# Kernel optimization log

Measured on AMD Instinct MI355X. Metric: run time of the kernel, lower is better.

## Reference

```python
import jax, jax.numpy as jnp
import numpy as np

B, CIN, D = 4096, 4, 8
EPS = 1e-5
NEG_SLOPE = 0.01


def _conv3d(x, w):
    # x: [B,C,D,H,W], w: [kD,kH,kW,Cin,Cout]
    return jax.lax.conv_general_dilated(
        x, w, window_strides=(1, 1, 1), padding='SAME',
        dimension_numbers=('NCDHW', 'DHWIO', 'NCDHW'))


def _bn(x, gamma, beta, mean, var):
    s = (1, -1) + (1,) * (x.ndim - 2)
    inv = gamma.reshape(s) / jnp.sqrt(var.reshape(s) + EPS)
    return (x - mean.reshape(s)) * inv + beta.reshape(s)


def _maxpool2(x):
    return jax.lax.reduce_window(x, -jnp.inf, jax.lax.max,
                                 (1, 1, 2, 2, 2), (1, 1, 2, 2, 2), 'VALID')


def setup_inputs() -> dict:
    key = jax.random.key(0)
    ks = jax.random.split(key, 16)
    mask = jax.random.randint(ks[0], (B, D, D, D), 0, 2).astype(bool)
    x = jax.random.normal(ks[1], (B, CIN, D, D, D), jnp.float32)
    x = x * mask[:, None].astype(jnp.float32)  # sparse tensor: zeros off active sites
    def he(k, shape, fan_in):
        return jax.random.normal(k, shape, jnp.float32) * (2.0 / fan_in) ** 0.5
    return {
        'x': x, 'mask': mask,
        'W1': he(ks[2], (3, 3, 3, CIN, 32), 27 * CIN),
        'g1': jnp.ones((32,)), 'b1': jnp.zeros((32,)),
        'm1': jax.random.normal(ks[3], (32,)) * 0.1,
        'v1': jax.random.uniform(ks[4], (32,), minval=0.5, maxval=1.5),
        'W2': he(ks[5], (3, 3, 3, 32, 64), 27 * 32),
        'g2': jnp.ones((64,)), 'b2': jnp.zeros((64,)),
        'm2': jax.random.normal(ks[6], (64,)) * 0.1,
        'v2': jax.random.uniform(ks[7], (64,), minval=0.5, maxval=1.5),
        'fcw1': he(ks[8], (128, 512), 512), 'fcb1': jnp.zeros((128,)),
        'fcw2': he(ks[9], (1, 128), 128), 'fcb2': jnp.zeros((1,)),
    }


def reference(x, mask, W1, g1, b1, m1, v1, W2, g2, b2, m2, v2, fcw1, fcb1, fcw2, fcb2):
    mf = mask.astype(x.dtype)[:, None]          # [B,1,8,8,8] active-site mask
    # SubMConv3d(CIN->32): conv restricted to active output sites
    h = _conv3d(x, W1) * mf
    h = jax.nn.relu(_bn(h, g1, b1, m1, v1) * mf)   # BN on active features only
    h = _maxpool2(h)                             # [B,32,4,4,4]
    mf2 = _maxpool2(mf)                          # active if any voxel in window active
    # SubMConv3d(32->64)
    h = _conv3d(h, W2) * mf2
    h = jax.nn.relu(_bn(h, g2, b2, m2, v2) * mf2)
    h = _maxpool2(h)                             # [B,64,2,2,2]
    h = h.reshape(h.shape[0], -1)                # [B,512]
    h = h @ fcw1.T + fcb1
    h = jnp.where(h >= 0, h, NEG_SLOPE * h)      # LeakyReLU
    # dropout: identity at inference
    return h @ fcw2.T + fcb2                     # [B,1]
```

## Files before the change

### kernel.cpp

```cpp
#include <hip/hip_runtime.h>
#include <hip/hip_bf16.h>

typedef unsigned short u16;
typedef unsigned int   u32;
typedef short bf16x8 __attribute__((ext_vector_type(8)));
typedef short bf16x4 __attribute__((ext_vector_type(4)));
typedef float f32x4  __attribute__((ext_vector_type(4)));

#define EPS 1e-5f

#define HBG_N   (4096 * 512)
#define W2B_OFF HBG_N
#define W1B_OFF (W2B_OFF + 55296)
#define FCW_OFF (W1B_OFF + 4096)

__device__ __forceinline__ u16 f2bf(float f) {
    __hip_bfloat16 h = __float2bfloat16(f);
    return *(const u16*)&h;
}

union BV { bf16x8 v; bf16x4 h[2]; };

__global__ __launch_bounds__(256) void prep_kernel(
        const float* __restrict__ W2, const float* __restrict__ W1,
        const float* __restrict__ fcw1, u16* __restrict__ ws) {
    int i = blockIdx.x * 256 + threadIdx.x;
    if (i < 55296) {
        int tap = i >> 11, rem = i & 2047;
        int co = rem >> 5, ci = rem & 31;
        ws[W2B_OFF + i] = f2bf(W2[(size_t)tap * 2048 + ci * 64 + co]);
    }
    if (i < 4096) {
        int j = i & 7, cout = (i >> 3) & 31, quad = (i >> 8) & 3, ks = i >> 10;
        int tap = ks * 8 + quad * 2 + (j >> 2), ci = j & 3;
        ws[W1B_OFF + i] = (tap < 27) ? f2bf(W1[tap * 128 + ci * 32 + cout]) : (u16)0;
    }
    if (i < 65536)
        ws[FCW_OFF + i] = f2bf(fcw1[i]);
}

__global__ __launch_bounds__(256) void conv_kernel(
        const float* __restrict__ x,    const u32*  __restrict__ mask,
        const float* __restrict__ g1,   const float* __restrict__ b1,
        const float* __restrict__ m1,   const float* __restrict__ v1,
        const float* __restrict__ g2,   const float* __restrict__ b2,
        const float* __restrict__ m2,   const float* __restrict__ v2,
        u16* __restrict__ ws) {

    const u16* w2b = ws + W2B_OFF;
    const u16* w1b = ws + W1B_OFF;

    __shared__ __align__(16) u16 xb[1000 * 4];
    __shared__ int   msk[512];
    __shared__ __align__(16) u16 act[216 * 40];
    __shared__ float mf2s[64];
    __shared__ float h2f[512];
    __shared__ float sc1s[32], sh1s[32], sc2s[64], sh2s[64];

    const int b = blockIdx.x;
    const int t = threadIdx.x;

    if (t < 32) {
        float sc = g1[t] / sqrtf(v1[t] + EPS);
        sc1s[t] = sc; sh1s[t] = b1[t] - m1[t] * sc;
    } else if (t < 96) {
        int c = t - 32;
        float sc = g2[c] / sqrtf(v2[c] + EPS);
        sc2s[c] = sc; sh2s[c] = b2[c] - m2[c] * sc;
    }
    for (int i = t; i < 2000; i += 256) ((u32*)xb)[i]  = 0u;
    for (int i = t; i < 4320; i += 256) ((u32*)act)[i] = 0u;
    __syncthreads();

    {
        const float* xp = x + (size_t)b * 2048;
        const u32*   mp = mask + (size_t)b * 512;
        for (int s = t; s < 512; s += 256) {
            float a0 = xp[s], a1 = xp[512 + s], a2 = xp[1024 + s], a3 = xp[1536 + s];
            int z = s >> 6, y = (s >> 3) & 7, xx = s & 7;
            int row = z * 100 + y * 10 + xx + 111;
            ((u32*)xb)[row * 2]     = (u32)f2bf(a0) | ((u32)f2bf(a1) << 16);
            ((u32*)xb)[row * 2 + 1] = (u32)f2bf(a2) | ((u32)f2bf(a3) << 16);
            msk[s] = (mp[s] != 0u);
        }
    }
    __syncthreads();

    const int lane = t & 63;
    const int n    = lane & 15;
    const int quad = lane >> 4;
    const int w    = __builtin_amdgcn_readfirstlane(t >> 6);

    {
        bf16x8 afr[4][2];
        #pragma unroll
        for (int ks = 0; ks < 4; ++ks)
            #pragma unroll
            for (int mt = 0; mt < 2; ++mt)
                afr[ks][mt] = *(const bf16x8*)(w1b +
                    (((ks * 4 + quad) * 32) + mt * 16 + n) * 8);

        int dA[8];
        #pragma unroll
        for (int q = 0; q < 8; ++q) {
            int tap = (q >> 1) * 8 + quad * 2 + (q & 1);
            int tc = (tap < 27) ? tap : 26;
            int kd = tc / 9, rr = tc - kd * 9, kh = rr / 3, kw = rr - kh * 3;
            dA[q] = (kd - 1) * 100 + (kh - 1) * 10 + (kw - 1);
        }

        const int py_ = n >> 2, px_ = n & 3;
        float pmax[8];
        #pragma unroll
        for (int j = 0; j < 8; ++j) pmax[j] = 0.f;
        int any = 0;

        #pragma unroll
        for (int i = 0; i < 8; ++i) {
            const int z  = 2 * w   + (i >> 2);
            const int y  = 2 * py_ + ((i >> 1) & 1);
            const int xx = 2 * px_ + (i & 1);
            const int sPad = z * 100 + y * 10 + xx + 111;

            f32x4 acc0 = (f32x4){0.f, 0.f, 0.f, 0.f};
            f32x4 acc1 = (f32x4){0.f, 0.f, 0.f, 0.f};

            #pragma unroll
            for (int ks = 0; ks < 4; ++ks) {
                BV bv;
                bv.h[0] = *(const bf16x4*)(xb + (sPad + dA[ks * 2])     * 4);
                bv.h[1] = *(const bf16x4*)(xb + (sPad + dA[ks * 2 + 1]) * 4);
                acc0 = __builtin_amdgcn_mfma_f32_16x16x32_bf16(afr[ks][0], bv.v, acc0, 0, 0, 0);
                acc1 = __builtin_amdgcn_mfma_f32_16x16x32_bf16(afr[ks][1], bv.v, acc1, 0, 0, 0);
            }

            const int mbit = msk[z * 64 + y * 8 + xx];
            const float mk = mbit ? 1.f : 0.f;
            any |= mbit;
            #pragma unroll
            for (int r = 0; r < 4; ++r) {
                int c0 = quad * 4 + r, c1 = 16 + quad * 4 + r;
                pmax[r]     = fmaxf(pmax[r],     fmaxf(acc0[r] * sc1s[c0] + sh1s[c0], 0.f) * mk);
                pmax[4 + r] = fmaxf(pmax[4 + r], fmaxf(acc1[r] * sc1s[c1] + sh1s[c1], 0.f) * mk);
            }
        }

        const int prow = (w + 1) * 36 + (py_ + 1) * 6 + (px_ + 1);
        #pragma unroll
        for (int mt = 0; mt < 2; ++mt) {
            u32 lo = (u32)f2bf(pmax[mt * 4])     | ((u32)f2bf(pmax[mt * 4 + 1]) << 16);
            u32 hi = (u32)f2bf(pmax[mt * 4 + 2]) | ((u32)f2bf(pmax[mt * 4 + 3]) << 16);
            ((u32*)act)[prow * 20 + mt * 8 + quad * 2]     = lo;
            ((u32*)act)[prow * 20 + mt * 8 + quad * 2 + 1] = hi;
        }
        if (quad == 0) mf2s[w * 16 + n] = any ? 1.f : 0.f;
    }
    __syncthreads();

    {
        const int nPad = ((n >> 2) + 1) * 6 + (n & 3) + 1;

        f32x4 acc[4];
        #pragma unroll
        for (int g = 0; g < 4; ++g) acc[g] = (f32x4){0.f, 0.f, 0.f, 0.f};

        #pragma unroll
        for (int kd = 0; kd < 3; ++kd) {
            #pragma unroll
            for (int kh = 0; kh < 3; ++kh) {
                #pragma unroll
                for (int kw = 0; kw < 3; ++kw) {
                    const int tap = (kd * 3 + kh) * 3 + kw;
                    bf16x8 afrag = *(const bf16x8*)(w2b + tap * 2048 + (w * 16 + n) * 32 + quad * 8);
                    #pragma unroll
                    for (int g = 0; g < 4; ++g) {
                        const int gp = g + kd - 1;
                        if (gp < 0 || gp > 3) continue;
                        const int C = (gp + 1) * 36 + (kh - 1) * 6 + (kw - 1);
                        bf16x8 bfrag = *(const bf16x8*)(act + (nPad + C) * 40 + quad * 8);
                        acc[g] = __builtin_amdgcn_mfma_f32_16x16x32_bf16(
                                     afrag, bfrag, acc[g], 0, 0, 0);
                    }
                }
            }
        }

        #pragma unroll
        for (int r = 0; r < 4; ++r) {
            const int cout = w * 16 + quad * 4 + r;
            float p2g[4];
            #pragma unroll
            for (int g = 0; g < 4; ++g) {
                const int site = g * 16 + n;
                float val = fmaxf(acc[g][r] * sc2s[cout] + sh2s[cout], 0.f) * mf2s[site];
                float p1 = fmaxf(val, __shfl_xor(val, 1, 64));
                p2g[g]   = fmaxf(p1,  __shfl_xor(p1, 4, 64));
            }
            if ((n & 5) == 0) {
                const int py = (n >> 3) & 1, px = (n >> 1) & 1;
                h2f[cout * 8 + 0 * 4 + py * 2 + px] = fmaxf(p2g[0], p2g[1]);
                h2f[cout * 8 + 1 * 4 + py * 2 + px] = fmaxf(p2g[2], p2g[3]);
            }
        }
    }
    __syncthreads();

    {
        u32 pk = (u32)f2bf(h2f[2 * t]) | ((u32)f2bf(h2f[2 * t + 1]) << 16);
        ((u32*)ws)[(size_t)b * 256 + t] = pk;
    }
}

__global__ __launch_bounds__(256) void fc_kernel(
        const u16* __restrict__ ws,
        const float* __restrict__ fcb1, const float* __restrict__ fcw2,
        const float* __restrict__ fcb2, float* __restrict__ out) {

    const u16* hbg   = ws;
    const u16* fcw1b = ws + FCW_OFF;

    __shared__ __align__(16) u16 abuf[32 * 520];
    __shared__ float fcpart[32][4];

    const int t = threadIdx.x;
    const int item0 = blockIdx.x * 32;

    {
        const int it = t >> 3, part = t & 7;
        const uint4* src = (const uint4*)(hbg + ((size_t)(item0 + it)) * 512 + part * 64);
        uint4* dst = (uint4*)(abuf + it * 520 + part * 64);
        #pragma unroll
        for (int c = 0; c < 8; ++c) dst[c] = src[c];
    }
    __syncthreads();

    const int lane = t & 63;
    const int n    = lane & 15;
    const int quad = lane >> 4;
    const int w    = __builtin_amdgcn_readfirstlane(t >> 6);
    const int jbase = w * 32;

    float fb1[2], fw2[2];
    #pragma unroll
    for (int nt = 0; nt < 2; ++nt) {
        fb1[nt] = fcb1[jbase + nt * 16 + n];
        fw2[nt] = fcw2[jbase + nt * 16 + n];
    }

    f32x4 acc[2][2];
    #pragma unroll
    for (int nt = 0; nt < 2; ++nt)
        #pragma unroll
        for (int mt = 0; mt < 2; ++mt) acc[nt][mt] = (f32x4){0.f, 0.f, 0.f, 0.f};

    #pragma unroll
    for (int ks = 0; ks < 16; ++ks) {
        bf16x8 bfr[2];
        #pragma unroll
        for (int nt = 0; nt < 2; ++nt)
            bfr[nt] = *(const bf16x8*)(fcw1b + (size_t)(jbase + nt * 16 + n) * 512 + ks * 32 + quad * 8);
        #pragma unroll
        for (int mt = 0; mt < 2; ++mt) {
            bf16x8 afr = *(const bf16x8*)(abuf + (mt * 16 + n) * 520 + ks * 32 + quad * 8);
            #pragma unroll
            for (int nt = 0; nt < 2; ++nt)
                acc[nt][mt] = __builtin_amdgcn_mfma_f32_16x16x32_bf16(
                                  afr, bfr[nt], acc[nt][mt], 0, 0, 0);
        }
    }

    #pragma unroll
    for (int mt = 0; mt < 2; ++mt) {
        #pragma unroll
        for (int r = 0; r < 4; ++r) {
            float s = 0.f;
            #pragma unroll
            for (int nt = 0; nt < 2; ++nt) {
                float y = acc[nt][mt][r] + fb1[nt];
                y = (y >= 0.f) ? y : 0.01f * y;
                s += y * fw2[nt];
            }
            s += __shfl_xor(s, 1, 64);
            s += __shfl_xor(s, 2, 64);
            s += __shfl_xor(s, 4, 64);
            s += __shfl_xor(s, 8, 64);
            if (n == 0) fcpart[mt * 16 + quad * 4 + r][w] = s;
        }
    }
    __syncthreads();
    if (t < 32)
        out[item0 + t] = fcpart[t][0] + fcpart[t][1] + fcpart[t][2] + fcpart[t][3] + fcb2[0];
}

extern "C" void kernel_launch(void* const* d_in, const int* in_sizes, int n_in,
                              void* d_out, int out_size, void* d_ws, size_t ws_size,
                              hipStream_t stream) {
    const float* x    = (const float*)d_in[0];
    const u32*   mask = (const u32*)d_in[1];
    const float* W1   = (const float*)d_in[2];
    const float* g1   = (const float*)d_in[3];
    const float* b1   = (const float*)d_in[4];
    const float* m1   = (const float*)d_in[5];
    const float* v1   = (const float*)d_in[6];
    const float* W2   = (const float*)d_in[7];
    const float* g2   = (const float*)d_in[8];
    const float* b2   = (const float*)d_in[9];
    const float* m2   = (const float*)d_in[10];
    const float* v2   = (const float*)d_in[11];
    const float* fcw1 = (const float*)d_in[12];
    const float* fcb1 = (const float*)d_in[13];
    const float* fcw2 = (const float*)d_in[14];
    const float* fcb2 = (const float*)d_in[15];
    u16*   ws  = (u16*)d_ws;
    float* out = (float*)d_out;

    prep_kernel<<<256, 256, 0, stream>>>(W2, W1, fcw1, ws);
    conv_kernel<<<4096, 256, 0, stream>>>(
        x, mask, g1, b1, m1, v1, g2, b2, m2, v2, ws);
    fc_kernel<<<128, 256, 0, stream>>>(ws, fcb1, fcw2, fcb2, out);
}
```

Measured before the change: 163.4 us.

## Double conv block to 512 threads and halve FC items per block

The conv kernel now runs 8 waves per sample instead of 4. For conv1, each wave handles one z-half of a pool window and the two halves are merged through shared memory with an extra barrier. For conv2, the waves are split by output-depth half, and the pooled mask is computed separately. The FC kernel handles 16 items per block across twice as many blocks. The aim is more parallel waves per sample to hide latency, at the cost of extra synchronisation, a read-modify-write max on shared memory, and possibly lower occupancy from the larger blocks.

```diff
diff --git a/kernel.cpp b/kernel.cpp
--- a/kernel.cpp
+++ b/kernel.cpp
@@ -39,7 +39,7 @@
         ws[FCW_OFF + i] = f2bf(fcw1[i]);
 }
 
-__global__ __launch_bounds__(256) void conv_kernel(
+__global__ __launch_bounds__(512) void conv_kernel(
         const float* __restrict__ x,    const u32*  __restrict__ mask,
         const float* __restrict__ g1,   const float* __restrict__ b1,
         const float* __restrict__ m1,   const float* __restrict__ v1,
@@ -68,28 +68,29 @@
         float sc = g2[c] / sqrtf(v2[c] + EPS);
         sc2s[c] = sc; sh2s[c] = b2[c] - m2[c] * sc;
     }
-    for (int i = t; i < 2000; i += 256) ((u32*)xb)[i]  = 0u;
-    for (int i = t; i < 4320; i += 256) ((u32*)act)[i] = 0u;
+    for (int i = t; i < 2000; i += 512) ((u32*)xb)[i]  = 0u;
+    for (int i = t; i < 4320; i += 512) ((u32*)act)[i] = 0u;
     __syncthreads();
 
     {
         const float* xp = x + (size_t)b * 2048;
         const u32*   mp = mask + (size_t)b * 512;
-        for (int s = t; s < 512; s += 256) {
-            float a0 = xp[s], a1 = xp[512 + s], a2 = xp[1024 + s], a3 = xp[1536 + s];
-            int z = s >> 6, y = (s >> 3) & 7, xx = s & 7;
-            int row = z * 100 + y * 10 + xx + 111;
-            ((u32*)xb)[row * 2]     = (u32)f2bf(a0) | ((u32)f2bf(a1) << 16);
-            ((u32*)xb)[row * 2 + 1] = (u32)f2bf(a2) | ((u32)f2bf(a3) << 16);
-            msk[s] = (mp[s] != 0u);
-        }
+        const int s = t;
+        float a0 = xp[s], a1 = xp[512 + s], a2 = xp[1024 + s], a3 = xp[1536 + s];
+        int z = s >> 6, y = (s >> 3) & 7, xx = s & 7;
+        int row = z * 100 + y * 10 + xx + 111;
+        ((u32*)xb)[row * 2]     = (u32)f2bf(a0) | ((u32)f2bf(a1) << 16);
+        ((u32*)xb)[row * 2 + 1] = (u32)f2bf(a2) | ((u32)f2bf(a3) << 16);
+        msk[s] = (mp[s] != 0u);
     }
     __syncthreads();
 
     const int lane = t & 63;
     const int n    = lane & 15;
     const int quad = lane >> 4;
-    const int w    = __builtin_amdgcn_readfirstlane(t >> 6);
+    const int w8   = __builtin_amdgcn_readfirstlane(t >> 6);
+    const int pz   = w8 & 3;
+    const int half = w8 >> 2;
 
     {
         bf16x8 afr[4][2];
@@ -110,17 +111,16 @@
         }
 
         const int py_ = n >> 2, px_ = n & 3;
+        const int zc  = 2 * pz + half;
         float pmax[8];
         #pragma unroll
         for (int j = 0; j < 8; ++j) pmax[j] = 0.f;
-        int any = 0;
-
-        #pragma unroll
-        for (int i = 0; i < 8; ++i) {
-            const int z  = 2 * w   + (i >> 2);
-            const int y  = 2 * py_ + ((i >> 1) & 1);
-            const int xx = 2 * px_ + (i & 1);
-            const int sPad = z * 100 + y * 10 + xx + 111;
+
+        #pragma unroll
+        for (int i4 = 0; i4 < 4; ++i4) {
+            const int y  = 2 * py_ + (i4 >> 1);
+            const int xx = 2 * px_ + (i4 & 1);
+            const int sPad = zc * 100 + y * 10 + xx + 111;
 
             f32x4 acc0 = (f32x4){0.f, 0.f, 0.f, 0.f};
             f32x4 acc1 = (f32x4){0.f, 0.f, 0.f, 0.f};
@@ -134,9 +134,7 @@
                 acc1 = __builtin_amdgcn_mfma_f32_16x16x32_bf16(afr[ks][1], bv.v, acc1, 0, 0, 0);
             }
 
-            const int mbit = msk[z * 64 + y * 8 + xx];
-            const float mk = mbit ? 1.f : 0.f;
-            any |= mbit;
+            const float mk = msk[zc * 64 + y * 8 + xx] ? 1.f : 0.f;
             #pragma unroll
             for (int r = 0; r < 4; ++r) {
                 int c0 = quad * 4 + r, c1 = 16 + quad * 4 + r;
@@ -145,24 +143,60 @@
             }
         }
 
-        const int prow = (w + 1) * 36 + (py_ + 1) * 6 + (px_ + 1);
-        #pragma unroll
-        for (int mt = 0; mt < 2; ++mt) {
-            u32 lo = (u32)f2bf(pmax[mt * 4])     | ((u32)f2bf(pmax[mt * 4 + 1]) << 16);
-            u32 hi = (u32)f2bf(pmax[mt * 4 + 2]) | ((u32)f2bf(pmax[mt * 4 + 3]) << 16);
-            ((u32*)act)[prow * 20 + mt * 8 + quad * 2]     = lo;
-            ((u32*)act)[prow * 20 + mt * 8 + quad * 2 + 1] = hi;
-        }
-        if (quad == 0) mf2s[w * 16 + n] = any ? 1.f : 0.f;
+        const int prow = (pz + 1) * 36 + (py_ + 1) * 6 + (px_ + 1);
+
+        if (half == 0) {
+            #pragma unroll
+            for (int mt = 0; mt < 2; ++mt) {
+                u32 lo = (u32)f2bf(pmax[mt * 4])     | ((u32)f2bf(pmax[mt * 4 + 1]) << 16);
+                u32 hi = (u32)f2bf(pmax[mt * 4 + 2]) | ((u32)f2bf(pmax[mt * 4 + 3]) << 16);
+                ((u32*)act)[prow * 20 + mt * 8 + quad * 2]     = lo;
+                ((u32*)act)[prow * 20 + mt * 8 + quad * 2 + 1] = hi;
+            }
+        }
+        __syncthreads();
+
+        if (half == 1) {
+            #pragma unroll
+            for (int mt = 0; mt < 2; ++mt) {
+                u32* p = ((u32*)act) + prow * 20 + mt * 8 + quad * 2;
+                u32 w0 = p[0], w1 = p[1];
+                float f0 = __uint_as_float(w0 << 16);
+                float f1 = __uint_as_float(w0 & 0xffff0000u);
+                float f2 = __uint_as_float(w1 << 16);
+                float f3 = __uint_as_float(w1 & 0xffff0000u);
+                f0 = fmaxf(f0, pmax[mt * 4 + 0]);
+                f1 = fmaxf(f1, pmax[mt * 4 + 1]);
+                f2 = fmaxf(f2, pmax[mt * 4 + 2]);
+                f3 = fmaxf(f3, pmax[mt * 4 + 3]);
+                p[0] = (u32)f2bf(f0) | ((u32)f2bf(f1) << 16);
+                p[1] = (u32)f2bf(f2) | ((u32)f2bf(f3) << 16);
+            }
+        }
+        if (t < 64) {
+            const int mz = t >> 4, my = (t >> 2) & 3, mx = t & 3;
+            int m = 0;
+            #pragma unroll
+            for (int dz = 0; dz < 2; ++dz)
+                #pragma unroll
+                for (int dy = 0; dy < 2; ++dy)
+                    #pragma unroll
+                    for (int dx = 0; dx < 2; ++dx)
+                        m |= msk[(2 * mz + dz) * 64 + (2 * my + dy) * 8 + (2 * mx + dx)];
+            mf2s[t] = m ? 1.f : 0.f;
+        }
     }
     __syncthreads();
 
     {
+        const int cw   = w8 & 3;
         const int nPad = ((n >> 2) + 1) * 6 + (n & 3) + 1;
-
-        f32x4 acc[4];
-        #pragma unroll
-        for (int g = 0; g < 4; ++g) acc[g] = (f32x4){0.f, 0.f, 0.f, 0.f};
+        const int rb0  = nPad + (2 * half) * 36;
+        const int rb1  = rb0 + 36;
+
+        f32x4 acc2[2];
+        acc2[0] = (f32x4){0.f, 0.f, 0.f, 0.f};
+        acc2[1] = (f32x4){0.f, 0.f, 0.f, 0.f};
 
         #pragma unroll
         for (int kd = 0; kd < 3; ++kd) {
@@ -171,15 +205,15 @@
                 #pragma unroll
                 for (int kw = 0; kw < 3; ++kw) {
                     const int tap = (kd * 3 + kh) * 3 + kw;
-                    bf16x8 afrag = *(const bf16x8*)(w2b + tap * 2048 + (w * 16 + n) * 32 + quad * 8);
-                    #pragma unroll
-                    for (int g = 0; g < 4; ++g) {
-                        const int gp = g + kd - 1;
-                        if (gp < 0 || gp > 3) continue;
-                        const int C = (gp + 1) * 36 + (kh - 1) * 6 + (kw - 1);
-                        bf16x8 bfrag = *(const bf16x8*)(act + (nPad + C) * 40 + quad * 8);
-                        acc[g] = __builtin_amdgcn_mfma_f32_16x16x32_bf16(
-                                     afrag, bfrag, acc[g], 0, 0, 0);
+                    bf16x8 afrag = *(const bf16x8*)(w2b + tap * 2048 + (cw * 16 + n) * 32 + quad * 8);
+                    const int C = kd * 36 + (kh - 1) * 6 + (kw - 1);
+                    if (!(kd == 0) || half != 0) {
+                        bf16x8 bfrag = *(const bf16x8*)(act + (rb0 + C) * 40 + quad * 8);
+                        acc2[0] = __builtin_amdgcn_mfma_f32_16x16x32_bf16(afrag, bfrag, acc2[0], 0, 0, 0);
+                    }
+                    if (!(kd == 2) || half != 1) {
+                        bf16x8 bfrag = *(const bf16x8*)(act + (rb1 + C) * 40 + quad * 8);
+                        acc2[1] = __builtin_amdgcn_mfma_f32_16x16x32_bf16(afrag, bfrag, acc2[1], 0, 0, 0);
                     }
                 }
             }
@@ -187,25 +221,24 @@
 
         #pragma unroll
         for (int r = 0; r < 4; ++r) {
-            const int cout = w * 16 + quad * 4 + r;
-            float p2g[4];
-            #pragma unroll
-            for (int g = 0; g < 4; ++g) {
-                const int site = g * 16 + n;
-                float val = fmaxf(acc[g][r] * sc2s[cout] + sh2s[cout], 0.f) * mf2s[site];
+            const int cout = cw * 16 + quad * 4 + r;
+            float p2g[2];
+            #pragma unroll
+            for (int gl = 0; gl < 2; ++gl) {
+                const int site = (2 * half + gl) * 16 + n;
+                float val = fmaxf(acc2[gl][r] * sc2s[cout] + sh2s[cout], 0.f) * mf2s[site];
                 float p1 = fmaxf(val, __shfl_xor(val, 1, 64));
-                p2g[g]   = fmaxf(p1,  __shfl_xor(p1, 4, 64));
+                p2g[gl]  = fmaxf(p1,  __shfl_xor(p1, 4, 64));
             }
             if ((n & 5) == 0) {
                 const int py = (n >> 3) & 1, px = (n >> 1) & 1;
-                h2f[cout * 8 + 0 * 4 + py * 2 + px] = fmaxf(p2g[0], p2g[1]);
-                h2f[cout * 8 + 1 * 4 + py * 2 + px] = fmaxf(p2g[2], p2g[3]);
-            }
-        }
-    }
-    __syncthreads();
-
-    {
+                h2f[cout * 8 + half * 4 + py * 2 + px] = fmaxf(p2g[0], p2g[1]);
+            }
+        }
+    }
+    __syncthreads();
+
+    if (t < 256) {
         u32 pk = (u32)f2bf(h2f[2 * t]) | ((u32)f2bf(h2f[2 * t + 1]) << 16);
         ((u32*)ws)[(size_t)b * 256 + t] = pk;
     }
@@ -219,18 +252,18 @@
     const u16* hbg   = ws;
     const u16* fcw1b = ws + FCW_OFF;
 
-    __shared__ __align__(16) u16 abuf[32 * 520];
-    __shared__ float fcpart[32][4];
+    __shared__ __align__(16) u16 abuf[16 * 520];
+    __shared__ float fcpart[16][4];
 
     const int t = threadIdx.x;
-    const int item0 = blockIdx.x * 32;
+    const int item0 = blockIdx.x * 16;
 
     {
-        const int it = t >> 3, part = t & 7;
-        const uint4* src = (const uint4*)(hbg + ((size_t)(item0 + it)) * 512 + part * 64);
-        uint4* dst = (uint4*)(abuf + it * 520 + part * 64);
-        #pragma unroll
-        for (int c = 0; c < 8; ++c) dst[c] = src[c];
+        const int it = t >> 4, part = t & 15;
+        const uint4* src = (const uint4*)(hbg + (size_t)(item0 + it) * 512 + part * 32);
+        uint4* dst = (uint4*)(abuf + it * 520 + part * 32);
+        #pragma unroll
+        for (int c = 0; c < 4; ++c) dst[c] = src[c];
     }
     __syncthreads();
 
@@ -247,48 +280,37 @@
         fw2[nt] = fcw2[jbase + nt * 16 + n];
     }
 
-    f32x4 acc[2][2];
-    #pragma unroll
-    for (int nt = 0; nt < 2; ++nt)
-        #pragma unroll
-        for (int mt = 0; mt < 2; ++mt) acc[nt][mt] = (f32x4){0.f, 0.f, 0.f, 0.f};
+    f32x4 acc[2];
+    acc[0] = (f32x4){0.f, 0.f, 0.f, 0.f};
+    acc[1] = (f32x4){0.f, 0.f, 0.f, 0.f};
 
     #pragma unroll
     for (int ks = 0; ks < 16; ++ks) {
-        bf16x8 bfr[2];
-        #pragma unroll
-        for (int nt = 0; nt < 2; ++nt)
-            bfr[nt] = *(const bf16x8*)(fcw1b + (size_t)(jbase + nt * 16 + n) * 512 + ks * 32 + quad * 8);
-        #pragma unroll
-        for (int mt = 0; mt < 2; ++mt) {
-            bf16x8 afr = *(const bf16x8*)(abuf + (mt * 16 + n) * 520 + ks * 32 + quad * 8);
-            #pragma unroll
-            for (int nt = 0; nt < 2; ++nt)
-                acc[nt][mt] = __builtin_amdgcn_mfma_f32_16x16x32_bf16(
-                                  afr, bfr[nt], acc[nt][mt], 0, 0, 0);
+        bf16x8 afr = *(const bf16x8*)(abuf + n * 520 + ks * 32 + quad * 8);
+        #pragma unroll
+        for (int nt = 0; nt < 2; ++nt) {
+            bf16x8 bfr = *(const bf16x8*)(fcw1b + (size_t)(jbase + nt * 16 + n) * 512 + ks * 32 + quad * 8);
+            acc[nt] = __builtin_amdgcn_mfma_f32_16x16x32_bf16(afr, bfr, acc[nt], 0, 0, 0);
         }
     }
 
     #pragma unroll
-    for (int mt = 0; mt < 2; ++mt) {
-        #pragma unroll
-        for (int r = 0; r < 4; ++r) {
-            float s = 0.f;
-            #pragma unroll
-            for (int nt = 0; nt < 2; ++nt) {
-                float y = acc[nt][mt][r] + fb1[nt];
-                y = (y >= 0.f) ? y : 0.01f * y;
-                s += y * fw2[nt];
-            }
-            s += __shfl_xor(s, 1, 64);
-            s += __shfl_xor(s, 2, 64);
-            s += __shfl_xor(s, 4, 64);
-            s += __shfl_xor(s, 8, 64);
-            if (n == 0) fcpart[mt * 16 + quad * 4 + r][w] = s;
-        }
-    }
-    __syncthreads();
-    if (t < 32)
+    for (int r = 0; r < 4; ++r) {
+        float s = 0.f;
+        #pragma unroll
+        for (int nt = 0; nt < 2; ++nt) {
+            float y = acc[nt][r] + fb1[nt];
+            y = (y >= 0.f) ? y : 0.01f * y;
+            s += y * fw2[nt];
+        }
+        s += __shfl_xor(s, 1, 64);
+        s += __shfl_xor(s, 2, 64);
+        s += __shfl_xor(s, 4, 64);
+        s += __shfl_xor(s, 8, 64);
+        if (n == 0) fcpart[quad * 4 + r][w] = s;
+    }
+    __syncthreads();
+    if (t < 16)
         out[item0 + t] = fcpart[t][0] + fcpart[t][1] + fcpart[t][2] + fcpart[t][3] + fcb2[0];
 }
 
@@ -315,7 +337,7 @@
     float* out = (float*)d_out;
 
     prep_kernel<<<256, 256, 0, stream>>>(W2, W1, fcw1, ws);
-    conv_kernel<<<4096, 256, 0, stream>>>(
+    conv_kernel<<<4096, 512, 0, stream>>>(
         x, mask, g1, b1, m1, v1, g2, b2, m2, v2, ws);
-    fc_kernel<<<128, 256, 0, stream>>>(ws, fcb1, fcw2, fcb2, out);
-}
+    fc_kernel<<<256, 256, 0, stream>>>(ws, fcb1, fcw2, fcb2, out);
+}
```

After: 187.5 us. 14.7% more time.

## Re-split conv2 work across waves for B-fragment reuse; halve FC block tile

Applied to the files above, without the earlier changes.

The second conv is re-partitioned so each wave computes two 16-channel output tiles over two z-planes instead of one channel tile over all four planes. Activation fragments for three z-slices are loaded once per (kh,kw) and reused across kd taps and both channel tiles, cutting LDS reads per MFMA. The FC kernel now processes 16 items per block instead of 32, doubling the grid for more parallelism at the cost of reloading the FC weights twice as often. LDS zero-fill is also widened to 128-bit stores.

```diff
diff --git a/kernel.cpp b/kernel.cpp
--- a/kernel.cpp
+++ b/kernel.cpp
@@ -39,6 +39,68 @@
         ws[FCW_OFF + i] = f2bf(fcw1[i]);
 }
 
+template<int G>
+__device__ __forceinline__ void conv2_part(
+        const u16* __restrict__ w2b, const u16* act,
+        const float* sc2s, const float* sh2s, const float* mf2s, float* h2f,
+        int n, int quad, int ctp) {
+
+    const int nPad = ((n >> 2) + 1) * 6 + (n & 3) + 1;
+    constexpr int z0 = (G == 0) ? 1 : 2;
+
+    f32x4 acc[2][2];
+    #pragma unroll
+    for (int ct = 0; ct < 2; ++ct)
+        #pragma unroll
+        for (int gl = 0; gl < 2; ++gl) acc[ct][gl] = (f32x4){0.f, 0.f, 0.f, 0.f};
+
+    #pragma unroll
+    for (int kh = 0; kh < 3; ++kh) {
+        #pragma unroll
+        for (int kw = 0; kw < 3; ++kw) {
+            bf16x8 bz[3];
+            #pragma unroll
+            for (int s = 0; s < 3; ++s)
+                bz[s] = *(const bf16x8*)(act +
+                    (nPad + (z0 + s) * 36 + (kh - 1) * 6 + (kw - 1)) * 40 + quad * 8);
+            #pragma unroll
+            for (int kd = 0; kd < 3; ++kd) {
+                const int tap = (kd * 3 + kh) * 3 + kw;
+                bf16x8 af0 = *(const bf16x8*)(w2b + tap * 2048 + ((ctp * 32 +  0) + n) * 32 + quad * 8);
+                bf16x8 af1 = *(const bf16x8*)(w2b + tap * 2048 + ((ctp * 32 + 16) + n) * 32 + quad * 8);
+                #pragma unroll
+                for (int gl = 0; gl < 2; ++gl) {
+                    const int zp = G + gl + kd;
+                    if (zp >= 1 && zp <= 4) {
+                        acc[0][gl] = __builtin_amdgcn_mfma_f32_16x16x32_bf16(af0, bz[zp - z0], acc[0][gl], 0, 0, 0);
+                        acc[1][gl] = __builtin_amdgcn_mfma_f32_16x16x32_bf16(af1, bz[zp - z0], acc[1][gl], 0, 0, 0);
+                    }
+                }
+            }
+        }
+    }
+
+    #pragma unroll
+    for (int r = 0; r < 4; ++r) {
+        #pragma unroll
+        for (int ct = 0; ct < 2; ++ct) {
+            const int cout = (ctp * 2 + ct) * 16 + quad * 4 + r;
+            float pz2[2];
+            #pragma unroll
+            for (int gl = 0; gl < 2; ++gl) {
+                const int site = (G + gl) * 16 + n;
+                float val = fmaxf(acc[ct][gl][r] * sc2s[cout] + sh2s[cout], 0.f) * mf2s[site];
+                float p1 = fmaxf(val, __shfl_xor(val, 1, 64));
+                pz2[gl]  = fmaxf(p1,  __shfl_xor(p1, 4, 64));
+            }
+            if ((n & 5) == 0) {
+                const int py = (n >> 3) & 1, px = (n >> 1) & 1;
+                h2f[cout * 8 + (G >> 1) * 4 + py * 2 + px] = fmaxf(pz2[0], pz2[1]);
+            }
+        }
+    }
+}
+
 __global__ __launch_bounds__(256) void conv_kernel(
         const float* __restrict__ x,    const u32*  __restrict__ mask,
         const float* __restrict__ g1,   const float* __restrict__ b1,
@@ -68,8 +130,11 @@
         float sc = g2[c] / sqrtf(v2[c] + EPS);
         sc2s[c] = sc; sh2s[c] = b2[c] - m2[c] * sc;
     }
-    for (int i = t; i < 2000; i += 256) ((u32*)xb)[i]  = 0u;
-    for (int i = t; i < 4320; i += 256) ((u32*)act)[i] = 0u;
+    {
+        const uint4 z4 = make_uint4(0u, 0u, 0u, 0u);
+        for (int i = t; i < 500;  i += 256) ((uint4*)xb)[i]  = z4;
+        for (int i = t; i < 1080; i += 256) ((uint4*)act)[i] = z4;
+    }
     __syncthreads();
 
     {
@@ -158,50 +223,11 @@
     __syncthreads();
 
     {
-        const int nPad = ((n >> 2) + 1) * 6 + (n & 3) + 1;
-
-        f32x4 acc[4];
-        #pragma unroll
-        for (int g = 0; g < 4; ++g) acc[g] = (f32x4){0.f, 0.f, 0.f, 0.f};
-
-        #pragma unroll
-        for (int kd = 0; kd < 3; ++kd) {
-            #pragma unroll
-            for (int kh = 0; kh < 3; ++kh) {
-                #pragma unroll
-                for (int kw = 0; kw < 3; ++kw) {
-                    const int tap = (kd * 3 + kh) * 3 + kw;
-                    bf16x8 afrag = *(const bf16x8*)(w2b + tap * 2048 + (w * 16 + n) * 32 + quad * 8);
-                    #pragma unroll
-                    for (int g = 0; g < 4; ++g) {
-                        const int gp = g + kd - 1;
-                        if (gp < 0 || gp > 3) continue;
-                        const int C = (gp + 1) * 36 + (kh - 1) * 6 + (kw - 1);
-                        bf16x8 bfrag = *(const bf16x8*)(act + (nPad + C) * 40 + quad * 8);
-                        acc[g] = __builtin_amdgcn_mfma_f32_16x16x32_bf16(
-                                     afrag, bfrag, acc[g], 0, 0, 0);
-                    }
-                }
-            }
-        }
-
-        #pragma unroll
-        for (int r = 0; r < 4; ++r) {
-            const int cout = w * 16 + quad * 4 + r;
-            float p2g[4];
-            #pragma unroll
-            for (int g = 0; g < 4; ++g) {
-                const int site = g * 16 + n;
-                float val = fmaxf(acc[g][r] * sc2s[cout] + sh2s[cout], 0.f) * mf2s[site];
-                float p1 = fmaxf(val, __shfl_xor(val, 1, 64));
-                p2g[g]   = fmaxf(p1,  __shfl_xor(p1, 4, 64));
-            }
-            if ((n & 5) == 0) {
-                const int py = (n >> 3) & 1, px = (n >> 1) & 1;
-                h2f[cout * 8 + 0 * 4 + py * 2 + px] = fmaxf(p2g[0], p2g[1]);
-                h2f[cout * 8 + 1 * 4 + py * 2 + px] = fmaxf(p2g[2], p2g[3]);
-            }
-        }
+        const int ctp = w & 1;
+        if ((w >> 1) == 0)
+            conv2_part<0>(w2b, act, sc2s, sh2s, mf2s, h2f, n, quad, ctp);
+        else
+            conv2_part<2>(w2b, act, sc2s, sh2s, mf2s, h2f, n, quad, ctp);
     }
     __syncthreads();
 
@@ -219,18 +245,18 @@
     const u16* hbg   = ws;
     const u16* fcw1b = ws + FCW_OFF;
 
-    __shared__ __align__(16) u16 abuf[32 * 520];
-    __shared__ float fcpart[32][4];
+    __shared__ __align__(16) u16 abuf[16 * 520];
+    __shared__ float fcpart[16][4];
 
     const int t = threadIdx.x;
-    const int item0 = blockIdx.x * 32;
-
-    {
-        const int it = t >> 3, part = t & 7;
-        const uint4* src = (const uint4*)(hbg + ((size_t)(item0 + it)) * 512 + part * 64);
-        uint4* dst = (uint4*)(abuf + it * 520 + part * 64);
-        #pragma unroll
-        for (int c = 0; c < 8; ++c) dst[c] = src[c];
+    const int item0 = blockIdx.x * 16;
+
+    {
+        const int it = t >> 4, part = t & 15;
+        const uint4* src = (const uint4*)(hbg + (size_t)(item0 + it) * 512 + part * 32);
+        uint4* dst = (uint4*)(abuf + it * 520 + part * 32);
+        #pragma unroll
+        for (int c = 0; c < 4; ++c) dst[c] = src[c];
     }
     __syncthreads();
 
@@ -247,48 +273,37 @@
         fw2[nt] = fcw2[jbase + nt * 16 + n];
     }
 
-    f32x4 acc[2][2];
-    #pragma unroll
-    for (int nt = 0; nt < 2; ++nt)
-        #pragma unroll
-        for (int mt = 0; mt < 2; ++mt) acc[nt][mt] = (f32x4){0.f, 0.f, 0.f, 0.f};
+    f32x4 acc[2];
+    acc[0] = (f32x4){0.f, 0.f, 0.f, 0.f};
+    acc[1] = (f32x4){0.f, 0.f, 0.f, 0.f};
 
     #pragma unroll
     for (int ks = 0; ks < 16; ++ks) {
-        bf16x8 bfr[2];
-        #pragma unroll
-        for (int nt = 0; nt < 2; ++nt)
-            bfr[nt] = *(const bf16x8*)(fcw1b + (size_t)(jbase + nt * 16 + n) * 512 + ks * 32 + quad * 8);
-        #pragma unroll
-        for (int mt = 0; mt < 2; ++mt) {
-            bf16x8 afr = *(const bf16x8*)(abuf + (mt * 16 + n) * 520 + ks * 32 + quad * 8);
-            #pragma unroll
-            for (int nt = 0; nt < 2; ++nt)
-                acc[nt][mt] = __builtin_amdgcn_mfma_f32_16x16x32_bf16(
-                                  afr, bfr[nt], acc[nt][mt], 0, 0, 0);
-        }
-    }
-
-    #pragma unroll
-    for (int mt = 0; mt < 2; ++mt) {
-        #pragma unroll
-        for (int r = 0; r < 4; ++r) {
-            float s = 0.f;
-            #pragma unroll
-            for (int nt = 0; nt < 2; ++nt) {
-                float y = acc[nt][mt][r] + fb1[nt];
-                y = (y >= 0.f) ? y : 0.01f * y;
-                s += y * fw2[nt];
-            }
-            s += __shfl_xor(s, 1, 64);
-            s += __shfl_xor(s, 2, 64);
-            s += __shfl_xor(s, 4, 64);
-            s += __shfl_xor(s, 8, 64);
-            if (n == 0) fcpart[mt * 16 + quad * 4 + r][w] = s;
-        }
-    }
-    __syncthreads();
-    if (t < 32)
+        bf16x8 afr = *(const bf16x8*)(abuf + n * 520 + ks * 32 + quad * 8);
+        #pragma unroll
+        for (int nt = 0; nt < 2; ++nt) {
+            bf16x8 bfr = *(const bf16x8*)(fcw1b + (size_t)(jbase + nt * 16 + n) * 512 + ks * 32 + quad * 8);
+            acc[nt] = __builtin_amdgcn_mfma_f32_16x16x32_bf16(afr, bfr, acc[nt], 0, 0, 0);
+        }
+    }
+
+    #pragma unroll
+    for (int r = 0; r < 4; ++r) {
+        float s = 0.f;
+        #pragma unroll
+        for (int nt = 0; nt < 2; ++nt) {
+            float y = acc[nt][r] + fb1[nt];
+            y = (y >= 0.f) ? y : 0.01f * y;
+            s += y * fw2[nt];
+        }
+        s += __shfl_xor(s, 1, 64);
+        s += __shfl_xor(s, 2, 64);
+        s += __shfl_xor(s, 4, 64);
+        s += __shfl_xor(s, 8, 64);
+        if (n == 0) fcpart[quad * 4 + r][w] = s;
+    }
+    __syncthreads();
+    if (t < 16)
         out[item0 + t] = fcpart[t][0] + fcpart[t][1] + fcpart[t][2] + fcpart[t][3] + fcb2[0];
 }
 
@@ -317,5 +332,5 @@
     prep_kernel<<<256, 256, 0, stream>>>(W2, W1, fcw1, ws);
     conv_kernel<<<4096, 256, 0, stream>>>(
         x, mask, g1, b1, m1, v1, g2, b2, m2, v2, ws);
-    fc_kernel<<<128, 256, 0, stream>>>(ws, fcb1, fcw2, fcb2, out);
-}
+    fc_kernel<<<256, 256, 0, stream>>>(ws, fcb1, fcw2, fcb2, out);
+}
```

Measured after the change: 181.0 us. +10.7%, slower.
